# Kernel optimization log

Measured on AMD Instinct MI355X. Metric: run time of the kernel, lower is better.

The kernel has to match this reference:

```python
import jax, jax.numpy as jnp
import numpy as np
from jax import lax

B, L, D = 2, 4096, 1024
H = 8
DK = D // H   # head_k_dim = 128
DV = D // H   # head_v_dim = 128
CONV_K = 4
CHUNK = 32
EPS = 1e-5


def _silu(x):
    return x * jax.nn.sigmoid(x)


def _causal_depthwise_conv_silu(x, w):
    """x: (b, l, ch); w: (ch, K). Causal depthwise conv1d followed by SiLU."""
    K = w.shape[1]
    l = x.shape[1]
    xp = jnp.pad(x, ((0, 0), (K - 1, 0), (0, 0)))
    y = sum(xp[:, i:i + l, :] * w[:, i] for i in range(K))
    return _silu(y)


def _l2norm(x):
    return x * lax.rsqrt(jnp.sum(x * x, axis=-1, keepdims=True) + 1e-12)


def _delta_rule_chunkwise(q, k, v, beta, chunk=CHUNK):
    """q,k: (b,h,l,dk); v: (b,h,l,dv); beta: (b,h,l). l % chunk == 0."""
    b, h, l, dk = q.shape
    dv = v.shape[-1]
    n = l // chunk
    q = _l2norm(q)
    k = _l2norm(k)
    v = v * beta[..., None]
    kb = k * beta[..., None]
    resh = lambda t: t.reshape(b, h, n, chunk, t.shape[-1])
    q, k, v, kb = map(resh, (q, k, v, kb))

    tri_strict = jnp.tril(jnp.ones((chunk, chunk), dtype=bool), -1)  # strictly lower
    attn = jnp.where(tri_strict, -(kb @ jnp.swapaxes(k, -1, -2)), 0.0)
    # UT transform: invert (I - strictly-lower) via forward substitution over chunk rows
    col = jnp.arange(chunk)
    for i in range(1, chunk):
        row = attn[..., i, :]                                    # (b,h,n,chunk)
        upd = jnp.einsum('bhnj,bhnjk->bhnk', row, attn)
        attn = attn.at[..., i, :].set(jnp.where(col < i, row + upd, row))
    attn = attn + jnp.eye(chunk, dtype=attn.dtype)

    u = attn @ v    # (b,h,n,chunk,dv)
    w = attn @ kb   # (b,h,n,chunk,dk)

    tri_incl = jnp.tril(jnp.ones((chunk, chunk), dtype=bool))  # incl. diagonal
    qc, kc, uc, wc = (jnp.moveaxis(t, 2, 0) for t in (q, k, u, w))

    def step(S, inp):
        qi, ki, ui, wi = inp  # each (b,h,chunk,d)
        attn_i = jnp.where(tri_incl, qi @ jnp.swapaxes(ki, -1, -2), 0.0)
        ui = ui - wi @ S
        oi = qi @ S + attn_i @ ui
        S = S + jnp.swapaxes(ki, -1, -2) @ ui
        return S, oi

    S0 = jnp.zeros((b, h, dk, dv), dtype=q.dtype)
    S, o = lax.scan(step, S0, (qc, kc, uc, wc))
    o = jnp.moveaxis(o, 0, 2).reshape(b, h, l, dv)
    return o, S


def setup_inputs() -> dict:
    key = jax.random.key(0)
    ks = jax.random.split(key, 10)
    s = 0.02
    return {
        'hidden_states': jax.random.normal(ks[0], (B, L, D), jnp.float32),
        'q_w': jax.random.normal(ks[1], (D, D), jnp.float32) * s,
        'k_w': jax.random.normal(ks[2], (D, D), jnp.float32) * s,
        'v_w': jax.random.normal(ks[3], (D, D), jnp.float32) * s,
        'conv_q_w': jax.random.normal(ks[4], (D, CONV_K), jnp.float32) * 0.3,
        'conv_k_w': jax.random.normal(ks[5], (D, CONV_K), jnp.float32) * 0.3,
        'conv_v_w': jax.random.normal(ks[6], (D, CONV_K), jnp.float32) * 0.3,
        'b_w': jax.random.normal(ks[7], (D, H), jnp.float32) * s,
        'mix_w': jax.random.normal(ks[8], (D, H), jnp.float32) * s,
        'mix_b': jnp.full((H,), -1.0, jnp.float32),      # mix_proj bias (init -1)
        'mix_bias': jnp.full((H,), -1.0, jnp.float32),   # extra learned mix bias
        'o_norm_w': jnp.ones((DV,), jnp.float32),
        'o_w': jax.random.normal(ks[9], (D, D), jnp.float32) * s,
    }


def reference(hidden_states, q_w, k_w, v_w, conv_q_w, conv_k_w, conv_v_w,
              b_w, mix_w, mix_b, mix_bias, o_norm_w, o_w):
    b, l, _ = hidden_states.shape
    # projections + causal short conv (SiLU activation, qk_activation='silu')
    q = _causal_depthwise_conv_silu(hidden_states @ q_w, conv_q_w)
    k = _causal_depthwise_conv_silu(hidden_states @ k_w, conv_k_w)
    v = _causal_depthwise_conv_silu(hidden_states @ v_w, conv_v_w)

    v_token = v.reshape(b, l, H, DV)
    q = q.reshape(b, l, H, DK)
    k = k.reshape(b, l, H, DK)

    beta = jax.nn.sigmoid(hidden_states @ b_w)  # (b,l,h)

    q_r = jnp.swapaxes(q, 1, 2)        # (b,h,l,dk)
    k_r = jnp.swapaxes(k, 1, 2)
    v_r = jnp.swapaxes(v_token, 1, 2)  # (b,h,l,dv)
    beta_r = jnp.swapaxes(beta, 1, 2)  # (b,h,l)

    o, _S = _delta_rule_chunkwise(q_r, k_r, v_r, beta_r)
    o = jnp.swapaxes(o, 1, 2)          # (b,l,h,dv)

    # bias-initialised adaptive mixing gate
    g = jax.nn.sigmoid(hidden_states @ mix_w + mix_b + mix_bias)[..., None]
    o = g * o + (1.0 - g) * v_token

    # per-head RMSNorm
    o = o * lax.rsqrt(jnp.mean(o * o, axis=-1, keepdims=True) + EPS) * o_norm_w

    o = o.reshape(b, l, H * DV) @ o_w
    return o
```

## Files before the change

### kernel.cpp

```cpp
#include <hip/hip_runtime.h>
#include <cstdint>
#include <cstddef>

typedef unsigned short u16;
typedef unsigned int u32;
typedef __attribute__((ext_vector_type(4))) u16 u16x4;
typedef __attribute__((ext_vector_type(8))) u16 u16x8;
typedef __attribute__((ext_vector_type(4))) float f32x4;
typedef __attribute__((ext_vector_type(8))) __bf16 bf16x8;

#define DEV static __device__ __forceinline__

DEV u16 f2bf(float f) {
  __bf16 h = (__bf16)f;
  return __builtin_bit_cast(u16, h);
}
DEV float bf2f(u16 s) { return __builtin_bit_cast(float, (u32)s << 16); }
DEV float sigm(float x) { return __builtin_amdgcn_rcpf(1.f + __expf(-x)); }

DEV void gl_lds16(const void* g, void* l) {
  __builtin_amdgcn_global_load_lds((const __attribute__((address_space(1))) u32*)g,
                                   (__attribute__((address_space(3))) u32*)l, 16, 0, 0);
}

constexpr int B_ = 2, L_ = 4096, H_ = 8;
constexpr int BL = B_ * L_;
constexpr int NC = L_ / 32;
constexpr int QKV_N = 3200;

constexpr int WOFF = 0;
constexpr int QOFF = 4096;
constexpr int KTOFF = 8192;
constexpr int AOFF = 12288;
constexpr int UTOFF = 13312;
constexpr int BLOB_ELEMS = 17408;

__global__ __launch_bounds__(256) void k_f32_to_bf16(const float* __restrict__ src,
                                                     u16* __restrict__ dst, int n4) {
  int i = blockIdx.x * 256 + threadIdx.x;
  if (i < n4) {
    f32x4 v = *(const f32x4*)(src + (size_t)i * 4);
    u16x4 o;
#pragma unroll
    for (int j = 0; j < 4; ++j) o[j] = f2bf(v[j]);
    *(u16x4*)(dst + (size_t)i * 4) = o;
  }
}

__global__ __launch_bounds__(256) void k_transpose_w(const float* __restrict__ s0, const float* __restrict__ s1,
                                                     const float* __restrict__ s2, const float* __restrict__ s3,
                                                     u16* __restrict__ d0, u16* __restrict__ d1,
                                                     u16* __restrict__ d2, u16* __restrict__ d3) {
  const float* src = blockIdx.z == 0 ? s0 : blockIdx.z == 1 ? s1 : blockIdx.z == 2 ? s2 : s3;
  u16* dst = blockIdx.z == 0 ? d0 : blockIdx.z == 1 ? d1 : blockIdx.z == 2 ? d2 : d3;
  __shared__ float tile[32][33];
  int k0 = blockIdx.y * 32, n0 = blockIdx.x * 32;
  int ty = threadIdx.x >> 5, tx = threadIdx.x & 31;
#pragma unroll
  for (int i = 0; i < 4; ++i)
    tile[ty + 8 * i][tx] = src[(size_t)(k0 + ty + 8 * i) * 1024 + n0 + tx];
  __syncthreads();
#pragma unroll
  for (int i = 0; i < 4; ++i) {
    int nl = ty + 8 * i;
    dst[(size_t)(n0 + nl) * 1024 + k0 + tx] = f2bf(tile[tx][nl]);
  }
}

__global__ __launch_bounds__(256) void k_pack_bg(const float* __restrict__ b_w, const float* __restrict__ mix_w,
                                                 u16* __restrict__ dst) {
  int idx = blockIdx.x * 256 + threadIdx.x;
  int r = idx >> 10, d = idx & 1023;
  float v = r < 8 ? b_w[d * 8 + r] : mix_w[d * 8 + (r - 8)];
  dst[(size_t)r * 1024 + d] = f2bf(v);
}

template<bool STORE_BF16>
__global__ __launch_bounds__(256) void gemm_bt(const u16* __restrict__ A, const u16* __restrict__ Bt,
                                               void* __restrict__ Cout, int M, int N, int K) {
  __shared__ u16 Ash[128 * 32];
  __shared__ u16 Bsh[128 * 32];
  const int tid = threadIdx.x;
  const int lane = tid & 63, w = tid >> 6;
  const int wr = w >> 1, wc = w & 1;
  const int g = lane >> 4, li = lane & 15;
  const int nbx = gridDim.x * gridDim.y;
  const int bid = blockIdx.y * gridDim.x + blockIdx.x;
  const int wg = (bid & 7) * (nbx >> 3) + (bid >> 3);
  const int mblk = (wg / gridDim.x) * 128, nblk = (wg % gridDim.x) * 128;
  const int srow = tid >> 2, sslot = tid & 3;

  f32x4 acc[4][4];
#pragma unroll
  for (int m = 0; m < 4; ++m)
#pragma unroll
    for (int n = 0; n < 4; ++n) acc[m][n] = (f32x4){0.f, 0.f, 0.f, 0.f};

  for (int kt = 0; kt < K; kt += 32) {
    __syncthreads();
#pragma unroll
    for (int half = 0; half < 2; ++half) {
      int row = srow + half * 64;
      int gk = kt + ((sslot ^ (row & 3)) << 3);
      gl_lds16(A + (size_t)(mblk + row) * K + gk, (char*)Ash + tid * 16 + half * 4096);
      gl_lds16(Bt + (size_t)(nblk + row) * K + gk, (char*)Bsh + tid * 16 + half * 4096);
    }
    __syncthreads();
    bf16x8 af[4], bfr[4];
#pragma unroll
    for (int m = 0; m < 4; ++m) {
      int row = wr * 64 + m * 16 + li;
      af[m] = *(const bf16x8*)&Ash[row * 32 + ((g ^ (li & 3)) << 3)];
    }
#pragma unroll
    for (int n = 0; n < 4; ++n) {
      int row = wc * 64 + n * 16 + li;
      bfr[n] = *(const bf16x8*)&Bsh[row * 32 + ((g ^ (li & 3)) << 3)];
    }
#pragma unroll
    for (int m = 0; m < 4; ++m)
#pragma unroll
      for (int n = 0; n < 4; ++n)
        acc[m][n] = __builtin_amdgcn_mfma_f32_16x16x32_bf16(af[m], bfr[n], acc[m][n], 0, 0, 0);
  }
#pragma unroll
  for (int m = 0; m < 4; ++m)
#pragma unroll
    for (int n = 0; n < 4; ++n)
#pragma unroll
      for (int r = 0; r < 4; ++r) {
        int grow = mblk + wr * 64 + m * 16 + g * 4 + r;
        int gcol = nblk + wc * 64 + n * 16 + li;
        if constexpr (STORE_BF16)
          ((u16*)Cout)[(size_t)grow * N + gcol] = f2bf(acc[m][n][r]);
        else
          ((float*)Cout)[(size_t)grow * N + gcol] = acc[m][n][r];
      }
}

__global__ __launch_bounds__(256) void k_conv(const u16* __restrict__ qkv,
                                              const float* __restrict__ cqw, const float* __restrict__ ckw,
                                              const float* __restrict__ cvw,
                                              const float* __restrict__ mix_b, const float* __restrict__ mix_bias,
                                              u16* __restrict__ qn, u16* __restrict__ kn, u16* __restrict__ kb,
                                              u16* __restrict__ vb, u16* __restrict__ vtok,
                                              float* __restrict__ gg) {
  const int blk = blockIdx.x;
  const int bh = blk >> 7, tile = blk & 127;
  const int b = bh >> 3, h = bh & 7;
  const int t0 = tile * 32;
  const int tid = threadIdx.x;
  __shared__ u16 lq[35 * 136], lk[35 * 136], lv[35 * 136];
  __shared__ float bval[32];

#pragma unroll
  for (int it = 0; it < 7; ++it) {
    int li = it * 256 + tid;
    if (li >= 1680) break;
    int strm = li / 560;
    int rem = li - strm * 560;
    int row = rem >> 4, e8 = rem & 15;
    int l = t0 - 3 + row;
    u16* dst = strm == 0 ? lq : strm == 1 ? lk : lv;
    u16x8 val = (u16x8){0, 0, 0, 0, 0, 0, 0, 0};
    if (l >= 0)
      val = *(const u16x8*)(qkv + (size_t)(b * L_ + l) * QKV_N + strm * 1024 + h * 128 + e8 * 8);
    *(u16x8*)&dst[row * 136 + e8 * 8] = val;
  }
  if (tid < 32) {
    int gt = b * L_ + t0 + tid;
    bval[tid] = sigm(bf2f(qkv[(size_t)gt * QKV_N + 3072 + h]));
    float gz = bf2f(qkv[(size_t)gt * QKV_N + 3080 + h]) + mix_b[h] + mix_bias[h];
    gg[gt * 8 + h] = sigm(gz);
  }
  __syncthreads();

  const int tok = tid >> 3, cg = tid & 7;
  const int l = t0 + tok;
  float aq[16], ak[16], av[16];

  auto do_stream = [&](const u16* lbuf, const float* wbase, float* acc) {
    u16x8 r0[4], r1[4];
#pragma unroll
    for (int i = 0; i < 4; ++i) {
      int base = (tok + i) * 136 + cg * 16;
      r0[i] = *(const u16x8*)&lbuf[base];
      r1[i] = *(const u16x8*)&lbuf[base + 8];
    }
#pragma unroll
    for (int e = 0; e < 8; ++e) {
      f32x4 w0 = *(const f32x4*)(wbase + e * 4);
      f32x4 w1 = *(const f32x4*)(wbase + (e + 8) * 4);
      float s0 = 0.f, s1 = 0.f;
#pragma unroll
      for (int i = 0; i < 4; ++i) {
        s0 += bf2f(r0[i][e]) * w0[i];
        s1 += bf2f(r1[i][e]) * w1[i];
      }
      acc[e] = s0;
      acc[e + 8] = s1;
    }
  };
  const int chb = (h * 128 + cg * 16) * 4;
  do_stream(lq, cqw + chb, aq);
  do_stream(lk, ckw + chb, ak);
  do_stream(lv, cvw + chb, av);

  float sq2 = 0.f, sk2 = 0.f;
#pragma unroll
  for (int e = 0; e < 16; ++e) {
    aq[e] = aq[e] * sigm(aq[e]);
    ak[e] = ak[e] * sigm(ak[e]);
    av[e] = av[e] * sigm(av[e]);
    sq2 += aq[e] * aq[e];
    sk2 += ak[e] * ak[e];
  }
#pragma unroll
  for (int m = 1; m <= 4; m <<= 1) {
    sq2 += __shfl_xor(sq2, m);
    sk2 += __shfl_xor(sk2, m);
  }
  float rq = rsqrtf(sq2 + 1e-12f), rk = rsqrtf(sk2 + 1e-12f);
  float bv = bval[tok];
  size_t hoff = ((size_t)bh * L_ + l) * 128 + cg * 16;
  size_t toff = ((size_t)(b * L_ + l)) * 1024 + h * 128 + cg * 16;
#pragma unroll
  for (int part = 0; part < 2; ++part) {
    u16x8 oq, ok, okb, ovb, ovt;
#pragma unroll
    for (int e = 0; e < 8; ++e) {
      float q = aq[part * 8 + e] * rq;
      float kk = ak[part * 8 + e] * rk;
      float vv = av[part * 8 + e];
      oq[e] = f2bf(q);
      ok[e] = f2bf(kk);
      okb[e] = f2bf(kk * bv);
      ovb[e] = f2bf(vv * bv);
      ovt[e] = f2bf(vv);
    }
    *(u16x8*)(qn + hoff + part * 8) = oq;
    *(u16x8*)(kn + hoff + part * 8) = ok;
    *(u16x8*)(kb + hoff + part * 8) = okb;
    *(u16x8*)(vb + hoff + part * 8) = ovb;
    *(u16x8*)(vtok + toff + part * 8) = ovt;
  }
}

__global__ __launch_bounds__(256) void k_chunkprep(const u16* __restrict__ qn, const u16* __restrict__ kn,
                                                   const u16* __restrict__ kb, const u16* __restrict__ vb,
                                                   u16* __restrict__ blob) {
  const int blk = blockIdx.x;
  const int bh = blk >> 7, ch = blk & 127;
  const int tid = threadIdx.x;
  __shared__ u16 kbl[32 * 136], knl[32 * 136], vbl[32 * 136], qnl[32 * 136];
  __shared__ float Af[32][33];
  __shared__ float X[32][33];
  __shared__ u16 w_s[4096], u_s[4096], attn_s[1024];
  size_t base = ((size_t)bh * L_ + (size_t)ch * 32) * 128;
#pragma unroll
  for (int rep = 0; rep < 2; ++rep) {
    int lin = rep * 2048 + tid * 8;
    int row = lin >> 7, col = lin & 127;
    *(u16x8*)&kbl[row * 136 + col] = *(const u16x8*)(kb + base + lin);
    *(u16x8*)&knl[row * 136 + col] = *(const u16x8*)(kn + base + lin);
    *(u16x8*)&vbl[row * 136 + col] = *(const u16x8*)(vb + base + lin);
    *(u16x8*)&qnl[row * 136 + col] = *(const u16x8*)(qn + base + lin);
  }
  __syncthreads();
  {
    const int i = tid >> 3;
    const int j0 = (tid & 7) * 4;
    float a[4] = {0, 0, 0, 0};
    float q[4] = {0, 0, 0, 0};
    for (int d8 = 0; d8 < 16; ++d8) {
      u16x8 kbv = *(const u16x8*)&kbl[i * 136 + d8 * 8];
      u16x8 qnv = *(const u16x8*)&qnl[i * 136 + d8 * 8];
#pragma unroll
      for (int jj = 0; jj < 4; ++jj) {
        u16x8 knv = *(const u16x8*)&knl[(j0 + jj) * 136 + d8 * 8];
#pragma unroll
        for (int e = 0; e < 8; ++e) {
          a[jj] += bf2f(kbv[e]) * bf2f(knv[e]);
          q[jj] += bf2f(qnv[e]) * bf2f(knv[e]);
        }
      }
    }
#pragma unroll
    for (int jj = 0; jj < 4; ++jj) {
      Af[i][j0 + jj] = a[jj];
      attn_s[i * 32 + j0 + jj] = f2bf((j0 + jj) <= i ? q[jj] : 0.f);
    }
  }
  __syncthreads();
  if (tid < 32) {
    int j = tid;
    for (int i = 0; i < 32; ++i) X[i][j] = (i == j) ? 1.f : 0.f;
    for (int i = j + 1; i < 32; ++i) {
      float s = 0.f;
      for (int m = j; m < i; ++m) s += Af[i][m] * X[m][j];
      X[i][j] = -s;
    }
  }
  __syncthreads();
  {
    const int i = tid >> 3;
    const int d0 = (tid & 7) * 16;
    float ua[16], wa[16];
#pragma unroll
    for (int dd = 0; dd < 16; ++dd) { ua[dd] = 0.f; wa[dd] = 0.f; }
    for (int m = 0; m <= i; ++m) {
      float xv = X[i][m];
      u16x8 v0 = *(const u16x8*)&vbl[m * 136 + d0];
      u16x8 v1 = *(const u16x8*)&vbl[m * 136 + d0 + 8];
      u16x8 k0 = *(const u16x8*)&kbl[m * 136 + d0];
      u16x8 k1 = *(const u16x8*)&kbl[m * 136 + d0 + 8];
#pragma unroll
      for (int e = 0; e < 8; ++e) {
        ua[e] += xv * bf2f(v0[e]);
        ua[8 + e] += xv * bf2f(v1[e]);
        wa[e] += xv * bf2f(k0[e]);
        wa[8 + e] += xv * bf2f(k1[e]);
      }
    }
#pragma unroll
    for (int part = 0; part < 2; ++part) {
      u16x8 su, sw;
#pragma unroll
      for (int e = 0; e < 8; ++e) {
        su[e] = f2bf(ua[part * 8 + e]);
        sw[e] = f2bf(wa[part * 8 + e]);
      }
      *(u16x8*)&u_s[i * 128 + d0 + part * 8] = su;
      *(u16x8*)&w_s[i * 128 + d0 + part * 8] = sw;
    }
  }
  __syncthreads();
  u16* bp = blob + (size_t)blk * BLOB_ELEMS;
#pragma unroll
  for (int it = 0; it < 2; ++it) {
    const int v8 = tid * 2 + it;
    const int f = v8 >> 6, l = v8 & 63;
    const int li = l & 15, g = l >> 4;
    {
      int mw = f >> 2, ks = f & 3;
      int row = mw * 16 + li, c0 = ks * 32 + g * 8;
      *(u16x8*)(bp + WOFF + (size_t)v8 * 8) = *(const u16x8*)&w_s[row * 128 + c0];
      *(u16x8*)(bp + QOFF + (size_t)v8 * 8) = *(const u16x8*)&qnl[row * 136 + c0];
    }
    {
      int dk = f * 16 + li, c0 = g * 8;
      u16x8 tv;
#pragma unroll
      for (int e = 0; e < 8; ++e) tv[e] = knl[(c0 + e) * 136 + dk];
      *(u16x8*)(bp + KTOFF + (size_t)v8 * 8) = tv;
    }
    {
      int smw = v8 >> 5, l0 = (v8 * 2) & 63;
      int s_ = smw >> 1, mw = smw & 1;
      u16x8 tv;
#pragma unroll
      for (int half = 0; half < 2; ++half) {
        int ll = l0 + half, lli = ll & 15, lg = ll >> 4;
#pragma unroll
        for (int r = 0; r < 4; ++r)
          tv[half * 4 + r] = u_s[(mw * 16 + lg * 4 + r) * 128 + s_ * 16 + lli];
      }
      *(u16x8*)(bp + UTOFF + (size_t)v8 * 8) = tv;
    }
  }
  if (tid < 128) {
    const int v8 = tid;
    const int mw = v8 >> 6, l = v8 & 63;
    const int li = l & 15, g = l >> 4;
    *(u16x8*)(bp + AOFF + (size_t)v8 * 8) = *(const u16x8*)&attn_s[(mw * 16 + li) * 32 + g * 8];
  }
}

struct Frags {
  bf16x8 aw[8], aq[8], akt[8], aat[2];
  u16x4 uv[2];
};

DEV void load_frags(Frags& f, const u16* __restrict__ bp, int lane, int sg) {
#pragma unroll
  for (int i = 0; i < 8; ++i)
    f.aw[i] = *(const bf16x8*)&bp[WOFF + ((size_t)(i * 64 + lane)) * 8];
#pragma unroll
  for (int mw = 0; mw < 2; ++mw)
    f.uv[mw] = *(const u16x4*)&bp[UTOFF + ((size_t)((sg * 2 + mw) * 64 + lane)) * 4];
#pragma unroll
  for (int i = 0; i < 8; ++i)
    f.aq[i] = *(const bf16x8*)&bp[QOFF + ((size_t)(i * 64 + lane)) * 8];
#pragma unroll
  for (int mw = 0; mw < 2; ++mw)
    f.aat[mw] = *(const bf16x8*)&bp[AOFF + ((size_t)(mw * 64 + lane)) * 8];
#pragma unroll
  for (int i = 0; i < 8; ++i)
    f.akt[i] = *(const bf16x8*)&bp[KTOFF + ((size_t)(i * 64 + lane)) * 8];
}

DEV void compute_chunk(const Frags& f, f32x4 (&S)[8], u16* st, u16* uft,
                       u16* __restrict__ o_out, size_t obase, int lane) {
  const int g = lane >> 4, li = lane & 15;
#pragma unroll
  for (int mi = 0; mi < 8; ++mi) {
    u16x4 sv;
#pragma unroll
    for (int r = 0; r < 4; ++r) sv[r] = f2bf(S[mi][r]);
    *(u16x4*)&st[li * 136 + mi * 16 + g * 4] = sv;
  }
  bf16x8 bS[4];
#pragma unroll
  for (int ks = 0; ks < 4; ++ks)
    bS[ks] = *(const bf16x8*)&st[li * 136 + ks * 32 + g * 8];

  f32x4 t1[2];
  t1[0] = (f32x4){0.f, 0.f, 0.f, 0.f};
  t1[1] = (f32x4){0.f, 0.f, 0.f, 0.f};
#pragma unroll
  for (int mw = 0; mw < 2; ++mw)
#pragma unroll
    for (int ks = 0; ks < 4; ++ks)
      t1[mw] = __builtin_amdgcn_mfma_f32_16x16x32_bf16(f.aw[mw * 4 + ks], bS[ks], t1[mw], 0, 0, 0);

#pragma unroll
  for (int mw = 0; mw < 2; ++mw) {
    u16x4 ufv;
#pragma unroll
    for (int r = 0; r < 4; ++r) ufv[r] = f2bf(bf2f(f.uv[mw][r]) - t1[mw][r]);
    *(u16x4*)&uft[li * 40 + mw * 16 + g * 4] = ufv;
  }
  bf16x8 bUF = *(const bf16x8*)&uft[li * 40 + g * 8];

  f32x4 oa[2];
  oa[0] = (f32x4){0.f, 0.f, 0.f, 0.f};
  oa[1] = (f32x4){0.f, 0.f, 0.f, 0.f};
#pragma unroll
  for (int mw = 0; mw < 2; ++mw)
#pragma unroll
    for (int ks = 0; ks < 4; ++ks)
      oa[mw] = __builtin_amdgcn_mfma_f32_16x16x32_bf16(f.aq[mw * 4 + ks], bS[ks], oa[mw], 0, 0, 0);
#pragma unroll
  for (int mw = 0; mw < 2; ++mw)
    oa[mw] = __builtin_amdgcn_mfma_f32_16x16x32_bf16(f.aat[mw], bUF, oa[mw], 0, 0, 0);

#pragma unroll
  for (int mw = 0; mw < 2; ++mw)
#pragma unroll
    for (int r = 0; r < 4; ++r)
      o_out[obase + (size_t)(mw * 16 + r) * 1024] = f2bf(oa[mw][r]);

#pragma unroll
  for (int mi = 0; mi < 8; ++mi)
    S[mi] = __builtin_amdgcn_mfma_f32_16x16x32_bf16(f.akt[mi], bUF, S[mi], 0, 0, 0);
}

__global__ __launch_bounds__(64, 1) void k_scan(const u16* __restrict__ blob, u16* __restrict__ o_out) {
  __shared__ u16 st[16 * 136];
  __shared__ u16 uft[16 * 40];
  const int bid = blockIdx.x;
  const int bh = (bid & 7) | ((bid >> 6) << 3);
  const int sg = (bid >> 3) & 7;
  const int b = bh >> 3, h = bh & 7;
  const int lane = threadIdx.x;
  const int g = lane >> 4, li = lane & 15;

  f32x4 S[8];
#pragma unroll
  for (int mi = 0; mi < 8; ++mi) S[mi] = (f32x4){0.f, 0.f, 0.f, 0.f};

  const u16* gb = blob + (size_t)bh * NC * BLOB_ELEMS;
  const size_t ob0 = ((size_t)b * L_ + g * 4) * 1024 + h * 128 + sg * 16 + li;

  Frags fa, fb;
  load_frags(fa, gb, lane, sg);
  for (int ch = 0; ch < NC - 2; ch += 2) {
    load_frags(fb, gb + (size_t)(ch + 1) * BLOB_ELEMS, lane, sg);
    compute_chunk(fa, S, st, uft, o_out, ob0 + (size_t)ch * 32 * 1024, lane);
    load_frags(fa, gb + (size_t)(ch + 2) * BLOB_ELEMS, lane, sg);
    compute_chunk(fb, S, st, uft, o_out, ob0 + (size_t)(ch + 1) * 32 * 1024, lane);
  }
  load_frags(fb, gb + (size_t)(NC - 1) * BLOB_ELEMS, lane, sg);
  compute_chunk(fa, S, st, uft, o_out, ob0 + (size_t)(NC - 2) * 32 * 1024, lane);
  compute_chunk(fb, S, st, uft, o_out, ob0 + (size_t)(NC - 1) * 32 * 1024, lane);
}

__global__ __launch_bounds__(256) void k_mixnorm(const u16* __restrict__ o_mid, const u16* __restrict__ vtok,
                                                 const float* __restrict__ g, const float* __restrict__ onw,
                                                 u16* __restrict__ omix) {
  int t = blockIdx.x, tid = threadIdx.x;
  int c = tid * 4, h = c >> 7, dk = c & 127;
  float gv = g[t * 8 + h];
  u16x4 ov = *(const u16x4*)(o_mid + (size_t)t * 1024 + c);
  u16x4 vv = *(const u16x4*)(vtok + (size_t)t * 1024 + c);
  float mx[4];
#pragma unroll
  for (int j = 0; j < 4; ++j) mx[j] = gv * bf2f(ov[j]) + (1.f - gv) * bf2f(vv[j]);
  float ss = mx[0] * mx[0] + mx[1] * mx[1] + mx[2] * mx[2] + mx[3] * mx[3];
#pragma unroll
  for (int m = 1; m <= 16; m <<= 1) ss += __shfl_xor(ss, m);
  float r = rsqrtf(ss * (1.f / 128.f) + 1e-5f);
  u16x4 oo;
#pragma unroll
  for (int j = 0; j < 4; ++j) oo[j] = f2bf(mx[j] * r * onw[dk + j]);
  *(u16x4*)(omix + (size_t)t * 1024 + c) = oo;
}

extern "C" void kernel_launch(void* const* d_in, const int* in_sizes, int n_in,
                              void* d_out, int out_size, void* d_ws, size_t ws_size,
                              hipStream_t stream) {
  const float* hidden = (const float*)d_in[0];
  const float* q_w = (const float*)d_in[1];
  const float* k_w = (const float*)d_in[2];
  const float* v_w = (const float*)d_in[3];
  const float* cqw = (const float*)d_in[4];
  const float* ckw = (const float*)d_in[5];
  const float* cvw = (const float*)d_in[6];
  const float* b_w = (const float*)d_in[7];
  const float* mix_w = (const float*)d_in[8];
  const float* mix_b = (const float*)d_in[9];
  const float* mix_bias = (const float*)d_in[10];
  const float* onw = (const float*)d_in[11];
  const float* o_w = (const float*)d_in[12];

  char* ws = (char*)d_ws;
  size_t off = 0;
  auto alloc = [&](size_t bytes) {
    char* p = ws + off;
    off += (bytes + 255) & ~(size_t)255;
    return p;
  };
  u16* hbf = (u16*)alloc(16777216);
  u16* wqkvT = (u16*)alloc((size_t)QKV_N * 1024 * 2);
  u16* woT = (u16*)alloc(2097152);
  float* gg = (float*)alloc(262144);
  u16* qn = (u16*)alloc(16777216);
  u16* kn = (u16*)alloc(16777216);
  u16* kbn = (u16*)alloc(16777216);
  u16* vbn = (u16*)alloc(16777216);
  u16* vtok = (u16*)alloc(16777216);
  u16* blob = (u16*)alloc(71303168);
  if (off > ws_size) return;

  u16* qkv = blob;
  u16* obuf = qn;

  k_f32_to_bf16<<<8192, 256, 0, stream>>>(hidden, hbf, 2097152);
  k_transpose_w<<<dim3(32, 32, 4), 256, 0, stream>>>(q_w, k_w, v_w, o_w,
                                                     wqkvT, wqkvT + 1024 * 1024,
                                                     wqkvT + 2 * 1024 * 1024, woT);
  k_pack_bg<<<64, 256, 0, stream>>>(b_w, mix_w, wqkvT + (size_t)3072 * 1024);
  gemm_bt<true><<<dim3(25, 64), 256, 0, stream>>>(hbf, wqkvT, qkv, BL, QKV_N, 1024);
  k_conv<<<2048, 256, 0, stream>>>(qkv, cqw, ckw, cvw, mix_b, mix_bias,
                                   qn, kn, kbn, vbn, vtok, gg);
  k_chunkprep<<<2048, 256, 0, stream>>>(qn, kn, kbn, vbn, blob);
  k_scan<<<128, 64, 0, stream>>>(blob, obuf);
  k_mixnorm<<<8192, 256, 0, stream>>>(obuf, vtok, gg, onw, hbf);
  gemm_bt<false><<<dim3(8, 64), 256, 0, stream>>>(hbf, woT, d_out, BL, 1024, 1024);
}
```

Measured before the change: 380.2 us.

## Rewrite chunk prep with MFMA Gram/UT products and blocked triangular inverse

Replaces the scalar FMA loops in the chunk-prep kernel with bf16 MFMA instructions: two waves compute the kb·kᵀ and q·kᵀ Gram matrices while the other waves write the kᵀ fragment layout. The 32x32 triangular inverse becomes two 16x16 diagonal-block forward substitutions plus a block off-diagonal product, and X·v / X·kb are computed with MFMA and written directly in fragment order. This targets scalar ALU and serial-loop cost in the prep stage. In exchange, X is rounded to bf16 before the products, which adds precision error.

After: 329.7 us. -13.3%, faster.

```diff
diff --git a/kernel.cpp b/kernel.cpp
--- a/kernel.cpp
+++ b/kernel.cpp
@@ -252,10 +252,15 @@
   const int blk = blockIdx.x;
   const int bh = blk >> 7, ch = blk & 127;
   const int tid = threadIdx.x;
+  const int wave = tid >> 6, lane = tid & 63;
+  const int g = lane >> 4, li = lane & 15;
   __shared__ u16 kbl[32 * 136], knl[32 * 136], vbl[32 * 136], qnl[32 * 136];
   __shared__ float Af[32][33];
-  __shared__ float X[32][33];
-  __shared__ u16 w_s[4096], u_s[4096], attn_s[1024];
+  __shared__ float Qs[32][33];
+  __shared__ float Xs[32][33];
+  __shared__ float Ts[16][17];
+  __shared__ u16 w_s[32 * 136];
+
   size_t base = ((size_t)bh * L_ + (size_t)ch * 32) * 128;
 #pragma unroll
   for (int rep = 0; rep < 2; ++rep) {
@@ -267,112 +272,152 @@
     *(u16x8*)&qnl[row * 136 + col] = *(const u16x8*)(qn + base + lin);
   }
   __syncthreads();
+
+  u16* bp = blob + (size_t)blk * BLOB_ELEMS;
+
+  if (wave < 2) {
+    const u16* asrc = (wave == 0) ? kbl : qnl;
+    bf16x8 a[2][4], bfr[2][4];
+#pragma unroll
+    for (int mt = 0; mt < 2; ++mt)
+#pragma unroll
+      for (int ks = 0; ks < 4; ++ks) {
+        a[mt][ks] = *(const bf16x8*)&asrc[(mt * 16 + li) * 136 + ks * 32 + g * 8];
+        bfr[mt][ks] = *(const bf16x8*)&knl[(mt * 16 + li) * 136 + ks * 32 + g * 8];
+      }
+    f32x4 acc[2][2];
+#pragma unroll
+    for (int mt = 0; mt < 2; ++mt)
+#pragma unroll
+      for (int nt = 0; nt < 2; ++nt) acc[mt][nt] = (f32x4){0.f, 0.f, 0.f, 0.f};
+#pragma unroll
+    for (int mt = 0; mt < 2; ++mt)
+#pragma unroll
+      for (int nt = 0; nt < 2; ++nt)
+#pragma unroll
+        for (int ks = 0; ks < 4; ++ks)
+          acc[mt][nt] = __builtin_amdgcn_mfma_f32_16x16x32_bf16(a[mt][ks], bfr[nt][ks], acc[mt][nt], 0, 0, 0);
+    if (wave == 0) {
+#pragma unroll
+      for (int mt = 0; mt < 2; ++mt)
+#pragma unroll
+        for (int nt = 0; nt < 2; ++nt)
+#pragma unroll
+          for (int r = 0; r < 4; ++r)
+            Af[mt * 16 + g * 4 + r][nt * 16 + li] = acc[mt][nt][r];
+    } else {
+#pragma unroll
+      for (int mt = 0; mt < 2; ++mt)
+#pragma unroll
+        for (int nt = 0; nt < 2; ++nt)
+#pragma unroll
+          for (int r = 0; r < 4; ++r) {
+            int row = mt * 16 + g * 4 + r, col = nt * 16 + li;
+            Qs[row][col] = (col <= row) ? acc[mt][nt][r] : 0.f;
+          }
+    }
+  } else {
+#pragma unroll
+    for (int it = 0; it < 4; ++it) {
+      int v8 = (tid - 128) * 4 + it;
+      int f = v8 >> 6, l = v8 & 63;
+      int lli = l & 15, lg = l >> 4;
+      int dk = f * 16 + lli;
+      u16x8 tv;
+#pragma unroll
+      for (int e = 0; e < 8; ++e) tv[e] = knl[(lg * 8 + e) * 136 + dk];
+      *(u16x8*)(bp + KTOFF + (size_t)v8 * 8) = tv;
+    }
+  }
+  __syncthreads();
+
+  if (wave == 0) {
+    if (lane < 32) {
+      for (int i = 0; i < 32; ++i) Xs[i][lane] = (i == lane) ? 1.f : 0.f;
+      int hb = lane >> 4, j = lane & 15, b0 = hb * 16;
+      for (int i = j + 1; i < 16; ++i) {
+        float s = 0.f;
+        for (int m = j; m < i; ++m) s += Af[b0 + i][b0 + m] * Xs[b0 + m][b0 + j];
+        Xs[b0 + i][b0 + j] = -s;
+      }
+    }
+    asm volatile("s_waitcnt lgkmcnt(0)" ::: "memory");
+#pragma unroll
+    for (int t = 0; t < 4; ++t) {
+      int idx = lane * 4 + t;
+      int i = idx >> 4, j = idx & 15;
+      float s = 0.f;
+      for (int m = 0; m < 16; ++m) s += Af[16 + i][m] * Xs[m][j];
+      Ts[i][j] = s;
+    }
+    asm volatile("s_waitcnt lgkmcnt(0)" ::: "memory");
+#pragma unroll
+    for (int t = 0; t < 4; ++t) {
+      int idx = lane * 4 + t;
+      int i = idx >> 4, j = idx & 15;
+      float s = 0.f;
+      for (int m = 0; m < 16; ++m) s += Xs[16 + i][16 + m] * Ts[m][j];
+      Xs[16 + i][j] = -s;
+    }
+  } else if (wave == 1) {
+#pragma unroll
+    for (int mw = 0; mw < 2; ++mw) {
+      u16x8 tv;
+#pragma unroll
+      for (int e = 0; e < 8; ++e) tv[e] = f2bf(Qs[mw * 16 + li][g * 8 + e]);
+      *(u16x8*)(bp + AOFF + (size_t)(mw * 64 + lane) * 8) = tv;
+    }
+  }
+  __syncthreads();
+
   {
-    const int i = tid >> 3;
-    const int j0 = (tid & 7) * 4;
-    float a[4] = {0, 0, 0, 0};
-    float q[4] = {0, 0, 0, 0};
-    for (int d8 = 0; d8 < 16; ++d8) {
-      u16x8 kbv = *(const u16x8*)&kbl[i * 136 + d8 * 8];
-      u16x8 qnv = *(const u16x8*)&qnl[i * 136 + d8 * 8];
-#pragma unroll
-      for (int jj = 0; jj < 4; ++jj) {
-        u16x8 knv = *(const u16x8*)&knl[(j0 + jj) * 136 + d8 * 8];
-#pragma unroll
-        for (int e = 0; e < 8; ++e) {
-          a[jj] += bf2f(kbv[e]) * bf2f(knv[e]);
-          q[jj] += bf2f(qnv[e]) * bf2f(knv[e]);
+    bf16x8 xa[2];
+#pragma unroll
+    for (int mw = 0; mw < 2; ++mw) {
+      u16x8 xv;
+#pragma unroll
+      for (int e = 0; e < 8; ++e) xv[e] = f2bf(Xs[mw * 16 + li][g * 8 + e]);
+      xa[mw] = __builtin_bit_cast(bf16x8, xv);
+    }
+    const u16* bsrc = (wave < 2) ? vbl : kbl;
+    const int wsel = wave & 1;
+#pragma unroll
+    for (int s4 = 0; s4 < 4; ++s4) {
+      int sg = wsel * 4 + s4;
+      u16x8 bv;
+#pragma unroll
+      for (int e = 0; e < 8; ++e) bv[e] = bsrc[(g * 8 + e) * 136 + sg * 16 + li];
+      bf16x8 bfrag = __builtin_bit_cast(bf16x8, bv);
+      f32x4 a0 = (f32x4){0.f, 0.f, 0.f, 0.f};
+      f32x4 a1 = (f32x4){0.f, 0.f, 0.f, 0.f};
+      a0 = __builtin_amdgcn_mfma_f32_16x16x32_bf16(xa[0], bfrag, a0, 0, 0, 0);
+      a1 = __builtin_amdgcn_mfma_f32_16x16x32_bf16(xa[1], bfrag, a1, 0, 0, 0);
+      if (wave < 2) {
+        u16x4 o0, o1;
+#pragma unroll
+        for (int r = 0; r < 4; ++r) { o0[r] = f2bf(a0[r]); o1[r] = f2bf(a1[r]); }
+        *(u16x4*)(bp + UTOFF + (size_t)((sg * 2 + 0) * 64 + lane) * 4) = o0;
+        *(u16x4*)(bp + UTOFF + (size_t)((sg * 2 + 1) * 64 + lane) * 4) = o1;
+      } else {
+#pragma unroll
+        for (int r = 0; r < 4; ++r) {
+          w_s[(0 * 16 + g * 4 + r) * 136 + sg * 16 + li] = f2bf(a0[r]);
+          w_s[(1 * 16 + g * 4 + r) * 136 + sg * 16 + li] = f2bf(a1[r]);
         }
       }
     }
-#pragma unroll
-    for (int jj = 0; jj < 4; ++jj) {
-      Af[i][j0 + jj] = a[jj];
-      attn_s[i * 32 + j0 + jj] = f2bf((j0 + jj) <= i ? q[jj] : 0.f);
-    }
   }
   __syncthreads();
-  if (tid < 32) {
-    int j = tid;
-    for (int i = 0; i < 32; ++i) X[i][j] = (i == j) ? 1.f : 0.f;
-    for (int i = j + 1; i < 32; ++i) {
-      float s = 0.f;
-      for (int m = j; m < i; ++m) s += Af[i][m] * X[m][j];
-      X[i][j] = -s;
-    }
-  }
-  __syncthreads();
-  {
-    const int i = tid >> 3;
-    const int d0 = (tid & 7) * 16;
-    float ua[16], wa[16];
-#pragma unroll
-    for (int dd = 0; dd < 16; ++dd) { ua[dd] = 0.f; wa[dd] = 0.f; }
-    for (int m = 0; m <= i; ++m) {
-      float xv = X[i][m];
-      u16x8 v0 = *(const u16x8*)&vbl[m * 136 + d0];
-      u16x8 v1 = *(const u16x8*)&vbl[m * 136 + d0 + 8];
-      u16x8 k0 = *(const u16x8*)&kbl[m * 136 + d0];
-      u16x8 k1 = *(const u16x8*)&kbl[m * 136 + d0 + 8];
-#pragma unroll
-      for (int e = 0; e < 8; ++e) {
-        ua[e] += xv * bf2f(v0[e]);
-        ua[8 + e] += xv * bf2f(v1[e]);
-        wa[e] += xv * bf2f(k0[e]);
-        wa[8 + e] += xv * bf2f(k1[e]);
-      }
-    }
-#pragma unroll
-    for (int part = 0; part < 2; ++part) {
-      u16x8 su, sw;
-#pragma unroll
-      for (int e = 0; e < 8; ++e) {
-        su[e] = f2bf(ua[part * 8 + e]);
-        sw[e] = f2bf(wa[part * 8 + e]);
-      }
-      *(u16x8*)&u_s[i * 128 + d0 + part * 8] = su;
-      *(u16x8*)&w_s[i * 128 + d0 + part * 8] = sw;
-    }
-  }
-  __syncthreads();
-  u16* bp = blob + (size_t)blk * BLOB_ELEMS;
+
 #pragma unroll
   for (int it = 0; it < 2; ++it) {
-    const int v8 = tid * 2 + it;
-    const int f = v8 >> 6, l = v8 & 63;
-    const int li = l & 15, g = l >> 4;
-    {
-      int mw = f >> 2, ks = f & 3;
-      int row = mw * 16 + li, c0 = ks * 32 + g * 8;
-      *(u16x8*)(bp + WOFF + (size_t)v8 * 8) = *(const u16x8*)&w_s[row * 128 + c0];
-      *(u16x8*)(bp + QOFF + (size_t)v8 * 8) = *(const u16x8*)&qnl[row * 136 + c0];
-    }
-    {
-      int dk = f * 16 + li, c0 = g * 8;
-      u16x8 tv;
-#pragma unroll
-      for (int e = 0; e < 8; ++e) tv[e] = knl[(c0 + e) * 136 + dk];
-      *(u16x8*)(bp + KTOFF + (size_t)v8 * 8) = tv;
-    }
-    {
-      int smw = v8 >> 5, l0 = (v8 * 2) & 63;
-      int s_ = smw >> 1, mw = smw & 1;
-      u16x8 tv;
-#pragma unroll
-      for (int half = 0; half < 2; ++half) {
-        int ll = l0 + half, lli = ll & 15, lg = ll >> 4;
-#pragma unroll
-        for (int r = 0; r < 4; ++r)
-          tv[half * 4 + r] = u_s[(mw * 16 + lg * 4 + r) * 128 + s_ * 16 + lli];
-      }
-      *(u16x8*)(bp + UTOFF + (size_t)v8 * 8) = tv;
-    }
-  }
-  if (tid < 128) {
-    const int v8 = tid;
-    const int mw = v8 >> 6, l = v8 & 63;
-    const int li = l & 15, g = l >> 4;
-    *(u16x8*)(bp + AOFF + (size_t)v8 * 8) = *(const u16x8*)&attn_s[(mw * 16 + li) * 32 + g * 8];
+    int v8 = tid * 2 + it;
+    int f = v8 >> 6, l = v8 & 63;
+    int lli = l & 15, lg = l >> 4;
+    int mw = f >> 2, ks = f & 3;
+    int row = mw * 16 + lli, c0 = ks * 32 + lg * 8;
+    *(u16x8*)(bp + WOFF + (size_t)v8 * 8) = *(const u16x8*)&w_s[row * 136 + c0];
+    *(u16x8*)(bp + QOFF + (size_t)v8 * 8) = *(const u16x8*)&qnl[row * 136 + c0];
   }
 }
 
```
